# Kernel tuning notes

Hardware: AMD Instinct MI355X
Metric: run time of the kernel (lower is better)

Reference implementation:

```python
import jax, jax.numpy as jnp
import numpy as np

N_NODES = 50000
N_EDGES = 800000
IN_FEATS = 128
HIDDEN = 64
EDGE_FEATS = 3


def setup_inputs() -> dict:
    key = jax.random.key(0)
    ks = jax.random.split(key, 8)
    s = lambda d: 1.0 / np.sqrt(d)
    return {
        "x": jax.random.normal(ks[0], (N_NODES, IN_FEATS), jnp.float32),
        "efeat": jax.random.normal(ks[1], (N_EDGES, EDGE_FEATS), jnp.float32),
        "src": jax.random.randint(ks[2], (N_EDGES,), 0, N_NODES, jnp.int32),
        "dst": jax.random.randint(ks[3], (N_EDGES,), 0, N_NODES, jnp.int32),
        "W1": jax.random.normal(ks[4], (IN_FEATS, HIDDEN), jnp.float32) * s(IN_FEATS),
        "b1": jnp.zeros((HIDDEN,), jnp.float32),
        "W2": jax.random.normal(ks[5], (HIDDEN, HIDDEN), jnp.float32) * s(HIDDEN),
        "b2": jnp.zeros((HIDDEN,), jnp.float32),
        "We": jax.random.normal(ks[6], (2 * HIDDEN + EDGE_FEATS, 1), jnp.float32) * s(2 * HIDDEN + EDGE_FEATS),
        "be": jnp.zeros((1,), jnp.float32),
    }


def reference(x, efeat, src, dst, W1, b1, W2, b2, We, be):
    n = x.shape[0]
    ones = jnp.ones(src.shape[0], x.dtype)
    # DGL GraphConv norm='both': scale src feats by out-deg^-1/2, aggregate, scale by in-deg^-1/2
    deg_out = jnp.clip(jax.ops.segment_sum(ones, src, num_segments=n), 1.0)
    deg_in = jnp.clip(jax.ops.segment_sum(ones, dst, num_segments=n), 1.0)
    c_src = deg_out ** -0.5  # [N]
    c_dst = deg_in ** -0.5   # [N]

    def graph_conv(h, W, b):
        hn = h * c_src[:, None]                             # pre-scale
        agg = jax.ops.segment_sum(hn[src], dst, num_segments=n)
        return (agg * c_dst[:, None]) @ W + b

    h = jax.nn.relu(graph_conv(x, W1, b1))
    h = graph_conv(h, W2, b2)

    # edge_func: sigmoid(Linear(cat[src_h, dst_h, efeat])) -- split We to avoid concat
    H = h.shape[1]
    Ws, Wd, Wf = We[:H], We[H:2 * H], We[2 * H:]
    logits = h[src] @ Ws + h[dst] @ Wd + efeat @ Wf + be   # [E, 1]
    return jax.nn.sigmoid(logits[:, 0])                    # [E]
```

## Files before the change

kernel.cpp:

```cpp
#include <hip/hip_runtime.h>
#include <math.h>
#include <stdint.h>

#define N_NODES 50000
#define N_EDGES 800000
#define IN_FEATS 128
#define HIDDEN 64

#define CSPLIT 32
#define CHUNK (N_EDGES / CSPLIT)
#define NQUART (N_NODES / 4)
#define NQWORDS (NQUART / 2)

typedef __attribute__((ext_vector_type(8))) short bf16x8;
typedef __attribute__((ext_vector_type(4))) float f32x4;

__device__ __forceinline__ unsigned short f2bf(float f) {
    unsigned u = __float_as_uint(f);
    u = (u + 0x7FFF + ((u >> 16) & 1)) >> 16;
    return (unsigned short)u;
}

__global__ __launch_bounds__(256) void hist2_kernel(const int* __restrict__ src,
                                                    const int* __restrict__ dst,
                                                    unsigned short* __restrict__ epos,
                                                    unsigned* __restrict__ pin,
                                                    unsigned* __restrict__ pout) {
    __shared__ unsigned cnt[NQWORDS];
    int b = blockIdx.x;
    int c = b >> 3;
    int kind = (b >> 2) & 1;
    int quar = b & 3;
    int lo = quar * NQUART;
    for (int i = threadIdx.x; i < NQWORDS; i += 256) cnt[i] = 0;
    __syncthreads();
    if (kind == 0) {
        const int4* d4 = reinterpret_cast<const int4*>(dst + c * CHUNK);
        for (int i = threadIdx.x; i < CHUNK / 4; i += 256) {
            int4 d = d4[i];
            int e = c * CHUNK + i * 4;
            unsigned u, old;
            u = (unsigned)(d.x - lo);
            if (u < NQUART) { old = atomicAdd(&cnt[u >> 1], 1u << ((u & 1) * 16));
                              epos[e + 0] = (unsigned short)(old >> ((u & 1) * 16)); }
            u = (unsigned)(d.y - lo);
            if (u < NQUART) { old = atomicAdd(&cnt[u >> 1], 1u << ((u & 1) * 16));
                              epos[e + 1] = (unsigned short)(old >> ((u & 1) * 16)); }
            u = (unsigned)(d.z - lo);
            if (u < NQUART) { old = atomicAdd(&cnt[u >> 1], 1u << ((u & 1) * 16));
                              epos[e + 2] = (unsigned short)(old >> ((u & 1) * 16)); }
            u = (unsigned)(d.w - lo);
            if (u < NQUART) { old = atomicAdd(&cnt[u >> 1], 1u << ((u & 1) * 16));
                              epos[e + 3] = (unsigned short)(old >> ((u & 1) * 16)); }
        }
    } else {
        const int4* s4 = reinterpret_cast<const int4*>(src + c * CHUNK);
        for (int i = threadIdx.x; i < CHUNK / 4; i += 256) {
            int4 s = s4[i];
            unsigned u;
            u = (unsigned)(s.x - lo); if (u < NQUART) atomicAdd(&cnt[u >> 1], 1u << ((u & 1) * 16));
            u = (unsigned)(s.y - lo); if (u < NQUART) atomicAdd(&cnt[u >> 1], 1u << ((u & 1) * 16));
            u = (unsigned)(s.z - lo); if (u < NQUART) atomicAdd(&cnt[u >> 1], 1u << ((u & 1) * 16));
            u = (unsigned)(s.w - lo); if (u < NQUART) atomicAdd(&cnt[u >> 1], 1u << ((u & 1) * 16));
        }
    }
    __syncthreads();
    unsigned* outp = (kind ? pout : pin) + c * (N_NODES / 2) + quar * NQWORDS;
    for (int i = threadIdx.x; i < NQWORDS; i += 256) outp[i] = cnt[i];
}

__global__ __launch_bounds__(256) void prep_kernel(const unsigned* __restrict__ pin,
                                                   const unsigned* __restrict__ pout,
                                                   float* __restrict__ cs,
                                                   float* __restrict__ cd,
                                                   int* __restrict__ offs,
                                                   int* __restrict__ bsum,
                                                   const float* __restrict__ W2,
                                                   const float* __restrict__ We,
                                                   const float* __restrict__ b2,
                                                   float* __restrict__ w2s,
                                                   float* __restrict__ w2d,
                                                   float* __restrict__ w2c) {
    int b = blockIdx.x;
    int t = threadIdx.x;
    if (b == 49) {
        if (t < 64) {
            float s = 0.f, d = 0.f;
            for (int j = 0; j < HIDDEN; ++j) {
                float w = W2[t * HIDDEN + j];
                s = fmaf(w, We[j], s);
                d = fmaf(w, We[HIDDEN + j], d);
            }
            w2s[t] = s;
            w2d[t] = d;
        } else if (t == 64) {
            float s = 0.f, d = 0.f;
            for (int j = 0; j < HIDDEN; ++j) {
                s = fmaf(We[j], b2[j], s);
                d = fmaf(We[HIDDEN + j], b2[j], d);
            }
            w2c[0] = s;
            w2c[1] = d;
        }
        return;
    }
    __shared__ int sums[256];
    int v0 = b * 1024 + t * 4;
    bool ok = v0 < N_NODES;
    unsigned si0 = 0, si1 = 0, si2 = 0, si3 = 0;
    unsigned so0 = 0, so1 = 0, so2 = 0, so3 = 0;
    if (ok) {
        int w0 = v0 >> 1;
#pragma unroll
        for (int c = 0; c < CSPLIT; ++c) {
            uint2 a = *reinterpret_cast<const uint2*>(pin + (size_t)c * (N_NODES / 2) + w0);
            uint2 o = *reinterpret_cast<const uint2*>(pout + (size_t)c * (N_NODES / 2) + w0);
            si0 += a.x & 0xffffu; si1 += a.x >> 16;
            si2 += a.y & 0xffffu; si3 += a.y >> 16;
            so0 += o.x & 0xffffu; so1 += o.x >> 16;
            so2 += o.y & 0xffffu; so3 += o.y >> 16;
        }
        *reinterpret_cast<float4*>(cs + v0) =
            make_float4(rsqrtf(fmaxf((float)so0, 1.f)), rsqrtf(fmaxf((float)so1, 1.f)),
                        rsqrtf(fmaxf((float)so2, 1.f)), rsqrtf(fmaxf((float)so3, 1.f)));
        *reinterpret_cast<float4*>(cd + v0) =
            make_float4(rsqrtf(fmaxf((float)si0, 1.f)), rsqrtf(fmaxf((float)si1, 1.f)),
                        rsqrtf(fmaxf((float)si2, 1.f)), rsqrtf(fmaxf((float)si3, 1.f)));
    }
    int d0 = (int)si0, d1 = (int)si1, d2 = (int)si2, d3 = (int)si3;
    sums[t] = d0 + d1 + d2 + d3;
    __syncthreads();
    for (int o = 1; o < 256; o <<= 1) {
        int v = (t >= o) ? sums[t - o] : 0;
        __syncthreads();
        sums[t] += v;
        __syncthreads();
    }
    int excl = (t == 0) ? 0 : sums[t - 1];
    if (ok) {
        *reinterpret_cast<int4*>(offs + v0) =
            make_int4(excl, excl + d0, excl + d0 + d1, excl + d0 + d1 + d2);
    }
    if (t == 255) bsum[b] = sums[255];
}

__global__ __launch_bounds__(256) void scan3_base_kernel(int* __restrict__ offs,
                                                         const int* __restrict__ bsum,
                                                         const unsigned* __restrict__ pin,
                                                         int* __restrict__ base) {
    __shared__ int sbase[64];
    int t = threadIdx.x;
    if (t < 64) {
        int val = (t < 49) ? bsum[t] : 0;
        int s = val;
#pragma unroll
        for (int o = 1; o < 64; o <<= 1) {
            int u = __shfl_up(s, o, 64);
            if (t >= o) s += u;
        }
        sbase[t] = s - val;
    }
    __syncthreads();
    int v = blockIdx.x * 256 + t;
    if (v >= N_NODES) return;
    int off = offs[v] + sbase[v >> 10];
    offs[v] = off;
    int run = off;
    int sh = (v & 1) * 16;
#pragma unroll
    for (int c = 0; c < CSPLIT; ++c) {
        base[(size_t)c * N_NODES + v] = run;
        run += (int)((pin[(size_t)c * (N_NODES / 2) + (v >> 1)] >> sh) & 0xffffu);
    }
    if (v == 0) offs[N_NODES] = N_EDGES;
}

__global__ __launch_bounds__(256) void fill_kernel(const int* __restrict__ src,
                                                   const int* __restrict__ dst,
                                                   const unsigned short* __restrict__ epos,
                                                   const int* __restrict__ base,
                                                   int* __restrict__ csr_src) {
    int t = blockIdx.x * 256 + threadIdx.x;
    int e0 = t * 4;
    if (e0 >= N_EDGES) return;
    int c = e0 / CHUNK;
    const int* basec = base + (size_t)c * N_NODES;
    int4 s = *reinterpret_cast<const int4*>(src + e0);
    int4 d = *reinterpret_cast<const int4*>(dst + e0);
    ushort4 ep = *reinterpret_cast<const ushort4*>(epos + e0);
    csr_src[basec[d.x] + ep.x] = s.x;
    csr_src[basec[d.y] + ep.y] = s.y;
    csr_src[basec[d.z] + ep.z] = s.z;
    csr_src[basec[d.w] + ep.w] = s.w;
}

__global__ __launch_bounds__(256) void gemm_mfma_kernel(const float* __restrict__ x,
                                                        const float* __restrict__ c_src,
                                                        const float* __restrict__ W,
                                                        unsigned short* __restrict__ yb) {
    __shared__ bf16x8 Bfrag[16][64];
    for (int idx = threadIdx.x; idx < 16 * 64; idx += 256) {
        int f = idx >> 6, l = idx & 63;
        int nt = f >> 2, kt = f & 3;
        int col = nt * 16 + (l & 15);
        int k0 = kt * 32 + (l >> 4) * 8;
        bf16x8 bv;
#pragma unroll
        for (int j = 0; j < 8; ++j) bv[j] = (short)f2bf(W[(k0 + j) * HIDDEN + col]);
        Bfrag[f][l] = bv;
    }
    __syncthreads();
    int wid = threadIdx.x >> 6, l = threadIdx.x & 63;
    bf16x8 Breg[16];
#pragma unroll
    for (int f = 0; f < 16; ++f) Breg[f] = Bfrag[f][l];

    int row0 = blockIdx.x * 64 + wid * 16;
    int arow = row0 + (l & 15);
    int asafe = min(arow, N_NODES - 1);
    const float* xr = x + (size_t)asafe * IN_FEATS + (l >> 4) * 8;
    f32x4 acc0 = {0.f, 0.f, 0.f, 0.f};
    f32x4 acc1 = {0.f, 0.f, 0.f, 0.f};
    f32x4 acc2 = {0.f, 0.f, 0.f, 0.f};
    f32x4 acc3 = {0.f, 0.f, 0.f, 0.f};
#pragma unroll
    for (int kt = 0; kt < 4; ++kt) {
        float4 a0 = *reinterpret_cast<const float4*>(xr + kt * 32);
        float4 a1 = *reinterpret_cast<const float4*>(xr + kt * 32 + 4);
        bf16x8 av;
        av[0] = (short)f2bf(a0.x); av[1] = (short)f2bf(a0.y);
        av[2] = (short)f2bf(a0.z); av[3] = (short)f2bf(a0.w);
        av[4] = (short)f2bf(a1.x); av[5] = (short)f2bf(a1.y);
        av[6] = (short)f2bf(a1.z); av[7] = (short)f2bf(a1.w);
        acc0 = __builtin_amdgcn_mfma_f32_16x16x32_bf16(av, Breg[0 * 4 + kt], acc0, 0, 0, 0);
        acc1 = __builtin_amdgcn_mfma_f32_16x16x32_bf16(av, Breg[1 * 4 + kt], acc1, 0, 0, 0);
        acc2 = __builtin_amdgcn_mfma_f32_16x16x32_bf16(av, Breg[2 * 4 + kt], acc2, 0, 0, 0);
        acc3 = __builtin_amdgcn_mfma_f32_16x16x32_bf16(av, Breg[3 * 4 + kt], acc3, 0, 0, 0);
    }
#pragma unroll
    for (int i = 0; i < 4; ++i) {
        int row = row0 + (l >> 4) * 4 + i;
        if (row < N_NODES) {
            float cs = c_src[row];
            unsigned short* yr = yb + (size_t)row * HIDDEN + (l & 15);
            yr[0]  = f2bf(acc0[i] * cs);
            yr[16] = f2bf(acc1[i] * cs);
            yr[32] = f2bf(acc2[i] * cs);
            yr[48] = f2bf(acc3[i] * cs);
        }
    }
}

__global__ __launch_bounds__(256) void gather_t_kernel(const unsigned short* __restrict__ y,
                                                       const int* __restrict__ offs,
                                                       const int* __restrict__ csr_src,
                                                       const float* __restrict__ c_src,
                                                       const float* __restrict__ c_dst,
                                                       const float* __restrict__ b1,
                                                       const float* __restrict__ w2s,
                                                       const float* __restrict__ w2d,
                                                       float2* __restrict__ t) {
    int wid = threadIdx.x >> 6, l = threadIdx.x & 63;
    int slot = l >> 3, q8 = l & 7;
    int v = blockIdx.x * 4 + wid;
    int beg = offs[v], end = offs[v + 1];
    float acc[8] = {0.f, 0.f, 0.f, 0.f, 0.f, 0.f, 0.f, 0.f};
    int k = beg;
    for (; k + 16 <= end; k += 16) {
        int sA = csr_src[k + slot];
        int sB = csr_src[k + 8 + slot];
        uint4 rA = *reinterpret_cast<const uint4*>(y + (size_t)sA * HIDDEN + q8 * 8);
        uint4 rB = *reinterpret_cast<const uint4*>(y + (size_t)sB * HIDDEN + q8 * 8);
        acc[0] += __uint_as_float(rA.x << 16);
        acc[1] += __uint_as_float(rA.x & 0xffff0000u);
        acc[2] += __uint_as_float(rA.y << 16);
        acc[3] += __uint_as_float(rA.y & 0xffff0000u);
        acc[4] += __uint_as_float(rA.z << 16);
        acc[5] += __uint_as_float(rA.z & 0xffff0000u);
        acc[6] += __uint_as_float(rA.w << 16);
        acc[7] += __uint_as_float(rA.w & 0xffff0000u);
        acc[0] += __uint_as_float(rB.x << 16);
        acc[1] += __uint_as_float(rB.x & 0xffff0000u);
        acc[2] += __uint_as_float(rB.y << 16);
        acc[3] += __uint_as_float(rB.y & 0xffff0000u);
        acc[4] += __uint_as_float(rB.z << 16);
        acc[5] += __uint_as_float(rB.z & 0xffff0000u);
        acc[6] += __uint_as_float(rB.w << 16);
        acc[7] += __uint_as_float(rB.w & 0xffff0000u);
    }
    if (k + 8 <= end) {
        int s = csr_src[k + slot];
        uint4 r = *reinterpret_cast<const uint4*>(y + (size_t)s * HIDDEN + q8 * 8);
        acc[0] += __uint_as_float(r.x << 16);
        acc[1] += __uint_as_float(r.x & 0xffff0000u);
        acc[2] += __uint_as_float(r.y << 16);
        acc[3] += __uint_as_float(r.y & 0xffff0000u);
        acc[4] += __uint_as_float(r.z << 16);
        acc[5] += __uint_as_float(r.z & 0xffff0000u);
        acc[6] += __uint_as_float(r.w << 16);
        acc[7] += __uint_as_float(r.w & 0xffff0000u);
        k += 8;
    }
    if (slot < end - k) {
        int s = csr_src[k + slot];
        uint4 r = *reinterpret_cast<const uint4*>(y + (size_t)s * HIDDEN + q8 * 8);
        acc[0] += __uint_as_float(r.x << 16);
        acc[1] += __uint_as_float(r.x & 0xffff0000u);
        acc[2] += __uint_as_float(r.y << 16);
        acc[3] += __uint_as_float(r.y & 0xffff0000u);
        acc[4] += __uint_as_float(r.z << 16);
        acc[5] += __uint_as_float(r.z & 0xffff0000u);
        acc[6] += __uint_as_float(r.w << 16);
        acc[7] += __uint_as_float(r.w & 0xffff0000u);
    }
#pragma unroll
    for (int i = 0; i < 8; ++i) {
        acc[i] += __shfl_xor(acc[i], 8, 64);
        acc[i] += __shfl_xor(acc[i], 16, 64);
        acc[i] += __shfl_xor(acc[i], 32, 64);
    }
    float c = c_dst[v];
    float4 ba = *reinterpret_cast<const float4*>(b1 + q8 * 8);
    float4 bb = *reinterpret_cast<const float4*>(b1 + q8 * 8 + 4);
    float4 wsa = *reinterpret_cast<const float4*>(w2s + q8 * 8);
    float4 wsb = *reinterpret_cast<const float4*>(w2s + q8 * 8 + 4);
    float4 wda = *reinterpret_cast<const float4*>(w2d + q8 * 8);
    float4 wdb = *reinterpret_cast<const float4*>(w2d + q8 * 8 + 4);
    float h0 = fmaxf(fmaf(c, acc[0], ba.x), 0.f);
    float h1 = fmaxf(fmaf(c, acc[1], ba.y), 0.f);
    float h2 = fmaxf(fmaf(c, acc[2], ba.z), 0.f);
    float h3 = fmaxf(fmaf(c, acc[3], ba.w), 0.f);
    float h4 = fmaxf(fmaf(c, acc[4], bb.x), 0.f);
    float h5 = fmaxf(fmaf(c, acc[5], bb.y), 0.f);
    float h6 = fmaxf(fmaf(c, acc[6], bb.z), 0.f);
    float h7 = fmaxf(fmaf(c, acc[7], bb.w), 0.f);
    float ps = h0 * wsa.x + h1 * wsa.y + h2 * wsa.z + h3 * wsa.w
             + h4 * wsb.x + h5 * wsb.y + h6 * wsb.z + h7 * wsb.w;
    float pd = h0 * wda.x + h1 * wda.y + h2 * wda.z + h3 * wda.w
             + h4 * wdb.x + h5 * wdb.y + h6 * wdb.z + h7 * wdb.w;
#pragma unroll
    for (int o = 1; o <= 4; o <<= 1) {
        ps += __shfl_xor(ps, o, 64);
        pd += __shfl_xor(pd, o, 64);
    }
    if (l == 0) {
        float cs = c_src[v];
        t[v] = make_float2(cs * ps, cs * pd);
    }
}

__global__ __launch_bounds__(256) void gather2_kernel(const float2* __restrict__ t,
                                                      const int* __restrict__ offs,
                                                      const int* __restrict__ csr_src,
                                                      const float* __restrict__ c_dst,
                                                      const float* __restrict__ w2c,
                                                      float* __restrict__ a_s,
                                                      float* __restrict__ a_d) {
    int wid = threadIdx.x >> 6, l = threadIdx.x & 63;
    int sub = l >> 4, q = l & 15;
    int v = blockIdx.x * 16 + wid * 4 + sub;
    int beg = offs[v], end = offs[v + 1];
    float ps = 0.f, pd = 0.f;
    for (int k = beg + q; k < end; k += 16) {
        float2 tv = t[csr_src[k]];
        ps += tv.x;
        pd += tv.y;
    }
#pragma unroll
    for (int o = 1; o <= 8; o <<= 1) {
        ps += __shfl_xor(ps, o, 64);
        pd += __shfl_xor(pd, o, 64);
    }
    if (q == 0) {
        float c = c_dst[v];
        a_s[v] = fmaf(c, ps, w2c[0]);
        a_d[v] = fmaf(c, pd, w2c[1]);
    }
}

__global__ __launch_bounds__(256) void edge_out_kernel(const int* __restrict__ src,
                                                       const int* __restrict__ dst,
                                                       const float* __restrict__ efeat,
                                                       const float* __restrict__ We,
                                                       const float* __restrict__ be,
                                                       const float* __restrict__ a_s,
                                                       const float* __restrict__ a_d,
                                                       float* __restrict__ out) {
    int t = blockIdx.x * 256 + threadIdx.x;
    int e0 = t * 4;
    if (e0 >= N_EDGES) return;
    float w0 = We[2 * HIDDEN + 0], w1 = We[2 * HIDDEN + 1], w2 = We[2 * HIDDEN + 2];
    float b = be[0];
    int4 s = *reinterpret_cast<const int4*>(src + e0);
    int4 d = *reinterpret_cast<const int4*>(dst + e0);
    const float4* f = reinterpret_cast<const float4*>(efeat + (long)e0 * 3);
    float4 f0 = f[0], f1 = f[1], f2 = f[2];
    float4 o;
    float z;
    z = a_s[s.x] + a_d[d.x] + f0.x * w0 + f0.y * w1 + f0.z * w2 + b;
    o.x = 1.0f / (1.0f + __expf(-z));
    z = a_s[s.y] + a_d[d.y] + f0.w * w0 + f1.x * w1 + f1.y * w2 + b;
    o.y = 1.0f / (1.0f + __expf(-z));
    z = a_s[s.z] + a_d[d.z] + f1.z * w0 + f1.w * w1 + f2.x * w2 + b;
    o.z = 1.0f / (1.0f + __expf(-z));
    z = a_s[s.w] + a_d[d.w] + f2.y * w0 + f2.z * w1 + f2.w * w2 + b;
    o.w = 1.0f / (1.0f + __expf(-z));
    *reinterpret_cast<float4*>(out + e0) = o;
}

extern "C" void kernel_launch(void* const* d_in, const int* in_sizes, int n_in,
                              void* d_out, int out_size, void* d_ws, size_t ws_size,
                              hipStream_t stream) {
    const float* x     = (const float*)d_in[0];
    const float* efeat = (const float*)d_in[1];
    const int*   src   = (const int*)d_in[2];
    const int*   dst   = (const int*)d_in[3];
    const float* W1    = (const float*)d_in[4];
    const float* b1    = (const float*)d_in[5];
    const float* W2    = (const float*)d_in[6];
    const float* b2    = (const float*)d_in[7];
    const float* We    = (const float*)d_in[8];
    const float* be    = (const float*)d_in[9];
    float* out = (float*)d_out;

    char* p = (char*)d_ws;
    auto alloc = [&](size_t bytes) {
        char* r = p;
        p += (bytes + 255) & ~(size_t)255;
        return r;
    };
    float* c_src   = (float*)alloc((size_t)N_NODES * 4);
    float* c_dst   = (float*)alloc((size_t)N_NODES * 4);
    float* a_s     = (float*)alloc((size_t)N_NODES * 4);
    float* a_d     = (float*)alloc((size_t)N_NODES * 4);
    int*   offs    = (int*)alloc((size_t)(N_NODES + 1) * 4);
    int*   bsum    = (int*)alloc(64 * 4);
    float* w2s     = (float*)alloc(HIDDEN * 4);
    float* w2d     = (float*)alloc(HIDDEN * 4);
    float* w2c     = (float*)alloc(2 * 4);
    unsigned*       pin   = (unsigned*)alloc((size_t)CSPLIT * (N_NODES / 2) * 4);
    unsigned*       pout  = (unsigned*)alloc((size_t)CSPLIT * (N_NODES / 2) * 4);
    unsigned short* epos  = (unsigned short*)alloc((size_t)N_EDGES * 2);
    int*            base  = (int*)alloc((size_t)CSPLIT * N_NODES * 4);
    int*            csr_src = (int*)alloc((size_t)N_EDGES * 4);
    unsigned short* yb    = (unsigned short*)alloc((size_t)N_NODES * HIDDEN * 2);
    float2*         t     = (float2*)alloc((size_t)N_NODES * 8);

    const int NB_V  = (N_NODES + 255) / 256;
    const int NB_E4 = (N_EDGES / 4 + 255) / 256;

    hist2_kernel<<<CSPLIT * 8, 256, 0, stream>>>(src, dst, epos, pin, pout);
    prep_kernel<<<50, 256, 0, stream>>>(pin, pout, c_src, c_dst, offs, bsum,
                                        W2, We, b2, w2s, w2d, w2c);
    scan3_base_kernel<<<NB_V, 256, 0, stream>>>(offs, bsum, pin, base);
    fill_kernel<<<NB_E4, 256, 0, stream>>>(src, dst, epos, base, csr_src);

    gemm_mfma_kernel<<<(N_NODES + 63) / 64, 256, 0, stream>>>(x, c_src, W1, yb);

    gather_t_kernel<<<N_NODES / 4, 256, 0, stream>>>(yb, offs, csr_src, c_src, c_dst,
                                                     b1, w2s, w2d, t);

    gather2_kernel<<<N_NODES / 16, 256, 0, stream>>>(t, offs, csr_src, c_dst, w2c, a_s, a_d);

    edge_out_kernel<<<NB_E4, 256, 0, stream>>>(src, dst, efeat, We, be, a_s, a_d, out);
}
```

Baseline: 102.3 us.

## Fuse CSR fill with feature GEMM and store per-chunk bases as 16-bit offsets

Merges the CSR fill kernel and the bf16 MFMA GEMM into one launch, with the leading blocks doing the edge scatter and the rest doing GEMM rows. This removes one launch and lets the two independent phases overlap. It also replaces the 32×N int base table with 16-bit offsets relative to offs, which halves that table's write and read traffic. In exchange the fill path now does an extra offs lookup per edge, and the 16-bit offsets assume per-node in-degree stays below 65536.

```diff
diff --git a/kernel.cpp b/kernel.cpp
--- a/kernel.cpp
+++ b/kernel.cpp
@@ -11,6 +11,9 @@
 #define CHUNK (N_EDGES / CSPLIT)
 #define NQUART (N_NODES / 4)
 #define NQWORDS (NQUART / 2)
+
+#define NB_E4 782
+#define NB_GEMM 782
 
 typedef __attribute__((ext_vector_type(8))) short bf16x8;
 typedef __attribute__((ext_vector_type(4))) float f32x4;
@@ -147,7 +150,7 @@
 __global__ __launch_bounds__(256) void scan3_base_kernel(int* __restrict__ offs,
                                                          const int* __restrict__ bsum,
                                                          const unsigned* __restrict__ pin,
-                                                         int* __restrict__ base) {
+                                                         unsigned short* __restrict__ baser) {
     __shared__ int sbase[64];
     int t = threadIdx.x;
     if (t < 64) {
@@ -165,40 +168,43 @@
     if (v >= N_NODES) return;
     int off = offs[v] + sbase[v >> 10];
     offs[v] = off;
-    int run = off;
+    int rel = 0;
     int sh = (v & 1) * 16;
 #pragma unroll
     for (int c = 0; c < CSPLIT; ++c) {
-        base[(size_t)c * N_NODES + v] = run;
-        run += (int)((pin[(size_t)c * (N_NODES / 2) + (v >> 1)] >> sh) & 0xffffu);
+        baser[(size_t)c * N_NODES + v] = (unsigned short)rel;
+        rel += (int)((pin[(size_t)c * (N_NODES / 2) + (v >> 1)] >> sh) & 0xffffu);
     }
     if (v == 0) offs[N_NODES] = N_EDGES;
 }
 
-__global__ __launch_bounds__(256) void fill_kernel(const int* __restrict__ src,
-                                                   const int* __restrict__ dst,
-                                                   const unsigned short* __restrict__ epos,
-                                                   const int* __restrict__ base,
-                                                   int* __restrict__ csr_src) {
-    int t = blockIdx.x * 256 + threadIdx.x;
-    int e0 = t * 4;
-    if (e0 >= N_EDGES) return;
-    int c = e0 / CHUNK;
-    const int* basec = base + (size_t)c * N_NODES;
-    int4 s = *reinterpret_cast<const int4*>(src + e0);
-    int4 d = *reinterpret_cast<const int4*>(dst + e0);
-    ushort4 ep = *reinterpret_cast<const ushort4*>(epos + e0);
-    csr_src[basec[d.x] + ep.x] = s.x;
-    csr_src[basec[d.y] + ep.y] = s.y;
-    csr_src[basec[d.z] + ep.z] = s.z;
-    csr_src[basec[d.w] + ep.w] = s.w;
-}
-
-__global__ __launch_bounds__(256) void gemm_mfma_kernel(const float* __restrict__ x,
+__global__ __launch_bounds__(256) void fill_gemm_kernel(const int* __restrict__ src,
+                                                        const int* __restrict__ dst,
+                                                        const unsigned short* __restrict__ epos,
+                                                        const int* __restrict__ offs,
+                                                        const unsigned short* __restrict__ baser,
+                                                        int* __restrict__ csr_src,
+                                                        const float* __restrict__ x,
                                                         const float* __restrict__ c_src,
                                                         const float* __restrict__ W,
                                                         unsigned short* __restrict__ yb) {
     __shared__ bf16x8 Bfrag[16][64];
+    if (blockIdx.x < NB_E4) {
+        int t = blockIdx.x * 256 + threadIdx.x;
+        int e0 = t * 4;
+        if (e0 >= N_EDGES) return;
+        int c = e0 / CHUNK;
+        const unsigned short* brc = baser + (size_t)c * N_NODES;
+        int4 s = *reinterpret_cast<const int4*>(src + e0);
+        int4 d = *reinterpret_cast<const int4*>(dst + e0);
+        ushort4 ep = *reinterpret_cast<const ushort4*>(epos + e0);
+        csr_src[offs[d.x] + brc[d.x] + ep.x] = s.x;
+        csr_src[offs[d.y] + brc[d.y] + ep.y] = s.y;
+        csr_src[offs[d.z] + brc[d.z] + ep.z] = s.z;
+        csr_src[offs[d.w] + brc[d.w] + ep.w] = s.w;
+        return;
+    }
+    int gb = blockIdx.x - NB_E4;
     for (int idx = threadIdx.x; idx < 16 * 64; idx += 256) {
         int f = idx >> 6, l = idx & 63;
         int nt = f >> 2, kt = f & 3;
@@ -215,7 +221,7 @@
 #pragma unroll
     for (int f = 0; f < 16; ++f) Breg[f] = Bfrag[f][l];
 
-    int row0 = blockIdx.x * 64 + wid * 16;
+    int row0 = gb * 64 + wid * 16;
     int arow = row0 + (l & 15);
     int asafe = min(arow, N_NODES - 1);
     const float* xr = x + (size_t)asafe * IN_FEATS + (l >> 4) * 8;
@@ -441,21 +447,20 @@
     unsigned*       pin   = (unsigned*)alloc((size_t)CSPLIT * (N_NODES / 2) * 4);
     unsigned*       pout  = (unsigned*)alloc((size_t)CSPLIT * (N_NODES / 2) * 4);
     unsigned short* epos  = (unsigned short*)alloc((size_t)N_EDGES * 2);
-    int*            base  = (int*)alloc((size_t)CSPLIT * N_NODES * 4);
+    unsigned short* baser = (unsigned short*)alloc((size_t)CSPLIT * N_NODES * 2);
     int*            csr_src = (int*)alloc((size_t)N_EDGES * 4);
     unsigned short* yb    = (unsigned short*)alloc((size_t)N_NODES * HIDDEN * 2);
     float2*         t     = (float2*)alloc((size_t)N_NODES * 8);
 
-    const int NB_V  = (N_NODES + 255) / 256;
-    const int NB_E4 = (N_EDGES / 4 + 255) / 256;
+    const int NB_V = (N_NODES + 255) / 256;
 
     hist2_kernel<<<CSPLIT * 8, 256, 0, stream>>>(src, dst, epos, pin, pout);
     prep_kernel<<<50, 256, 0, stream>>>(pin, pout, c_src, c_dst, offs, bsum,
                                         W2, We, b2, w2s, w2d, w2c);
-    scan3_base_kernel<<<NB_V, 256, 0, stream>>>(offs, bsum, pin, base);
-    fill_kernel<<<NB_E4, 256, 0, stream>>>(src, dst, epos, base, csr_src);
-
-    gemm_mfma_kernel<<<(N_NODES + 63) / 64, 256, 0, stream>>>(x, c_src, W1, yb);
+    scan3_base_kernel<<<NB_V, 256, 0, stream>>>(offs, bsum, pin, baser);
+
+    fill_gemm_kernel<<<NB_E4 + NB_GEMM, 256, 0, stream>>>(src, dst, epos, offs, baser,
+                                                          csr_src, x, c_src, W1, yb);
 
     gather_t_kernel<<<N_NODES / 4, 256, 0, stream>>>(yb, offs, csr_src, c_src, c_dst,
                                                      b1, w2s, w2d, t);
```

After: 100.3 us. 1.02x faster.
